# Kernel tuning notes

Hardware: AMD Instinct MI355X
Metric: run time of the kernel (lower is better)

Reference implementation:

```python
import jax, jax.numpy as jnp
import numpy as np

B, N, E, H = 2, 1000, 2000, 128


def setup_inputs() -> dict:
    key = jax.random.key(0)
    k1, k2, k3, k4, k5 = jax.random.split(key, 5)
    node_state = jax.random.normal(k1, (B, N, H), dtype=jnp.float32)
    edge_vec = jax.random.normal(k2, (B, E, H), dtype=jnp.float32)
    node2edge = jax.random.uniform(k3, (B, E, N), dtype=jnp.float32)
    edge2node = jax.random.uniform(k4, (B, N, E), dtype=jnp.float32)
    # xavier_uniform for a (H, H, H) tensor: fan_in = H*H, fan_out = H (torch views last 2 dims)
    bound = float(np.sqrt(6.0 / (H + H * H)))
    edge_network = jax.random.uniform(k5, (H, H, H), dtype=jnp.float32, minval=-bound, maxval=bound)
    return {
        "node_state": node_state,
        "edge_vec": edge_vec,
        "node2edge": node2edge,
        "edge2node": edge2node,
        "edge_network": edge_network,
    }


def reference(node_state, edge_vec, node2edge, edge2node, edge_network):
    # node2edge_emb[b,e,h] = sum_n node2edge[b,e,n] * node_state[b,n,h]
    n2e_emb = jnp.einsum("ben,bnh->beh", node2edge, node_state)
    # per-edge dynamic weight W[b,e,i,j] = sum_h edge_vec[b,e,h] * edge_network[h,i,j],
    # applied to n2e_emb; fused into one contraction (grouped edge-conditioned conv).
    new_n2e = jnp.einsum("beh,hij,bej->bei", edge_vec, edge_network, n2e_emb)
    norm = jnp.sum(edge2node, axis=2, keepdims=True) + 1.0  # [B,N,1]
    agg = (jnp.einsum("bne,bei->bni", edge2node, new_n2e) + node_state) / norm
    return agg
```

## Files before the change

### kernel.cpp

```cpp
#include <hip/hip_runtime.h>
#include <hip/hip_bf16.h>
#include <stdint.h>

#define Bv 2
#define Nv 1000
#define Ev 2000
#define Hv 128

typedef __attribute__((ext_vector_type(8))) short bf16x8;
typedef __attribute__((ext_vector_type(4))) float f32x4;
typedef unsigned short u16;
typedef unsigned int u32;

static __device__ __forceinline__ u32 pack2bf(float a, float b) {
  union { __hip_bfloat162 h; u32 u; } c;
  c.h = __float22bfloat162_rn(make_float2(a, b));
  return c.u;
}
static __device__ __forceinline__ u16 cvt1bf(float a) {
  return (u16)(pack2bf(a, 0.f) & 0xffffu);
}

static __device__ __forceinline__ void gload_lds16(const void* g, void* l) {
  __builtin_amdgcn_global_load_lds(
      (const __attribute__((address_space(1))) void*)g,
      (__attribute__((address_space(3))) void*)l, 16, 0, 0);
}

__global__ void k_prep(const float* __restrict__ en, u16* __restrict__ enbf,
                       const float* __restrict__ ns, u16* __restrict__ nsT) {
  const int bid = blockIdx.x;
  const int t = threadIdx.x;
  if (bid < 1024) {
    size_t idx = ((size_t)bid * 256u + t) * 8u;
    const f32x4* p = (const f32x4*)(en + idx);
    f32x4 a = p[0], b = p[1];
    uint4 o;
    o.x = pack2bf(a.x, a.y);
    o.y = pack2bf(a.z, a.w);
    o.z = pack2bf(b.x, b.y);
    o.w = pack2bf(b.z, b.w);
    *(uint4*)(enbf + idx) = o;
  } else {
    __shared__ float tile[32][33];
    const int zb = bid - 1024;
    const int x = zb & 31, y = (zb >> 5) & 3, z = zb >> 7;
    const float* src = ns + (size_t)z * Nv * Hv;
    u16* dst = nsT + (size_t)z * Hv * 1024;
    const int r0 = x * 32, c0 = y * 32;
    const int tx = t & 31, ty = t >> 5;
#pragma unroll
    for (int rr = 0; rr < 4; ++rr) {
      int r = r0 + ty + rr * 8;
      int c = c0 + tx;
      float v = (r < Nv) ? src[(size_t)r * Hv + c] : 0.f;
      tile[ty + rr * 8][tx] = v;
    }
    __syncthreads();
#pragma unroll
    for (int rr = 0; rr < 4; ++rr) {
      int oc = c0 + ty + rr * 8;
      int orr = r0 + tx;
      dst[(size_t)oc * 1024 + orr] = cvt1bf(tile[tx][ty + rr * 8]);
    }
  }
}

template <int M, int KREAL, int KPAD, int NKC, int NMT, bool ROWSUM>
__launch_bounds__(256, 4)
__global__ void k_gemm_flat(const float* __restrict__ A, const u16* __restrict__ BT,
                            float* __restrict__ Cpart, float* __restrict__ nrmpart) {
  __shared__ u16 AL[64 * 136];
  __shared__ float rowsum[64];
  const int id = blockIdx.x;
  const int kcid = id % NKC;
  const int mt = (id / NKC) % NMT;
  const int b = id / (NKC * NMT);
  A     += (size_t)b * M * KREAL;
  BT    += (size_t)b * 128 * KPAD;
  Cpart += (size_t)kcid * (2 * M * 128) + (size_t)b * M * 128;
  if (ROWSUM) nrmpart += (size_t)kcid * (2 * M) + (size_t)b * M;
  const int t = threadIdx.x;
  const int lane = t & 63;
  const int w = t >> 6;
  const int row16 = lane & 15;
  const int kg = lane >> 4;
  const int mrow0 = mt * 64;
  const int kc = kcid * 128;
  const int mtg = (w >> 1) * 2;
  const int itg = (w & 1) * 4;
  f32x4 acc[2][4];
#pragma unroll
  for (int i = 0; i < 2; ++i)
#pragma unroll
    for (int j = 0; j < 4; ++j) acc[i][j] = (f32x4){0.f, 0.f, 0.f, 0.f};
  if (ROWSUM && t < 64) rowsum[t] = 0.f;
  __syncthreads();
#pragma unroll
  for (int r = 0; r < 4; ++r) {
    const int chunk = t + r * 256;
    const int m = chunk >> 4;
    const int jc = (chunk & 15) * 8;
    const int gm = mrow0 + m;
    const int gk = kc + jc;
    f32x4 x0 = {0.f, 0.f, 0.f, 0.f}, x1 = {0.f, 0.f, 0.f, 0.f};
    if (gm < M && gk + 8 <= KREAL) {
      const f32x4* p = (const f32x4*)(A + (size_t)gm * KREAL + gk);
      x0 = p[0];
      x1 = p[1];
    }
    if (ROWSUM) {
      float s8 = x0.x + x0.y + x0.z + x0.w + x1.x + x1.y + x1.z + x1.w;
      s8 += __shfl_down(s8, 8, 16);
      s8 += __shfl_down(s8, 4, 16);
      s8 += __shfl_down(s8, 2, 16);
      s8 += __shfl_down(s8, 1, 16);
      if ((lane & 15) == 0) rowsum[m] += s8;
    }
    uint4 o;
    o.x = pack2bf(x0.x, x0.y);
    o.y = pack2bf(x0.z, x0.w);
    o.z = pack2bf(x1.x, x1.y);
    o.w = pack2bf(x1.z, x1.w);
    *(uint4*)&AL[m * 136 + jc] = o;
  }
  __syncthreads();
#pragma unroll
  for (int kk = 0; kk < 4; ++kk) {
    bf16x8 a[2], bfr[4];
#pragma unroll
    for (int q = 0; q < 2; ++q)
      a[q] = *(const bf16x8*)&AL[((mtg + q) * 16 + row16) * 136 + kk * 32 + kg * 8];
#pragma unroll
    for (int q = 0; q < 4; ++q)
      bfr[q] = *(const bf16x8*)(BT + (size_t)((itg + q) * 16 + row16) * KPAD + kc + kk * 32 + kg * 8);
#pragma unroll
    for (int mi = 0; mi < 2; ++mi)
#pragma unroll
      for (int ii = 0; ii < 4; ++ii)
        acc[mi][ii] = __builtin_amdgcn_mfma_f32_16x16x32_bf16(a[mi], bfr[ii], acc[mi][ii], 0, 0, 0);
  }
  if (ROWSUM && t < 64 && mrow0 + t < M) nrmpart[mrow0 + t] = rowsum[t];
#pragma unroll
  for (int mi = 0; mi < 2; ++mi) {
#pragma unroll
    for (int r = 0; r < 4; ++r) {
      const int lrow = (mtg + mi) * 16 + kg * 4 + r;
      const int gm = mrow0 + lrow;
      if (gm < M) {
#pragma unroll
        for (int ii = 0; ii < 4; ++ii)
          Cpart[(size_t)gm * 128 + (itg + ii) * 16 + row16] = acc[mi][ii][r];
      }
    }
  }
}

__global__ void k_reduce_emb(const float* __restrict__ part, float* __restrict__ emb) {
  const int idx = blockIdx.x * 256 + threadIdx.x;
  const f32x4* p = (const f32x4*)part + idx;
  f32x4 s = {0.f, 0.f, 0.f, 0.f};
#pragma unroll
  for (int kc = 0; kc < 8; ++kc) s += p[(size_t)kc * 128000];
  ((f32x4*)emb)[idx] = s;
}

__global__ void k_cvt_red(const float* __restrict__ part2, u16* __restrict__ neweT) {
  const int tid = blockIdx.x * 256 + threadIdx.x;
  const size_t f0 = (size_t)tid * 8;
  const int m0 = (int)(f0 & 2047);
  uint4 o;
  if (m0 >= Ev) {
    o = make_uint4(0, 0, 0, 0);
  } else {
    const f32x4* p = (const f32x4*)(part2 + f0);
    f32x4 s0 = {0.f, 0.f, 0.f, 0.f}, s1 = {0.f, 0.f, 0.f, 0.f};
#pragma unroll
    for (int hg = 0; hg < 8; ++hg) {
      s0 += p[(size_t)hg * 131072];
      s1 += p[(size_t)hg * 131072 + 1];
    }
    o.x = pack2bf(s0.x, s0.y);
    o.y = pack2bf(s0.z, s0.w);
    o.z = pack2bf(s1.x, s1.y);
    o.w = pack2bf(s1.z, s1.w);
  }
  *(uint4*)(neweT + f0) = o;
}

__global__ void k_epi_red(const float* __restrict__ part3, const float* __restrict__ nrmp,
                          const float* __restrict__ ns, float* __restrict__ out) {
  const int tid = blockIdx.x * 256 + threadIdx.x;
  const size_t f0 = (size_t)tid * 4;
  const int row = (int)(f0 >> 7);
  const f32x4* p = (const f32x4*)(part3 + f0);
  f32x4 s = {0.f, 0.f, 0.f, 0.f};
#pragma unroll
  for (int kc = 0; kc < 16; ++kc) s += p[(size_t)kc * 64000];
  float nm = 1.0f;
#pragma unroll
  for (int kc = 0; kc < 16; ++kc) nm += nrmp[(size_t)kc * 2000 + row];
  f32x4 nsv = *(const f32x4*)(ns + f0);
  *(f32x4*)(out + f0) = (s + nsv) * (1.0f / nm);
}

__launch_bounds__(256, 2)
__global__ void k_edge_mix(const float* __restrict__ ev, const float* __restrict__ emb,
                           const u16* __restrict__ enbf, float* __restrict__ part2) {
  __shared__ u16 APL[2][16384];
  __shared__ float EVL[64 * 20];
  const int id = blockIdx.x;
  const int hgrp = id & 7;
  const int rest = id >> 3;
  const int mt = rest & 31;
  const int b = rest >> 5;
  const int h0 = hgrp * 16;
  const int t = threadIdx.x;
  const int lane = t & 63;
  const int w = t >> 6;
  const int row16 = lane & 15;
  const int kg = lane >> 4;
  const int mbase = mt * 64;

  if (t < 64) {
    const int ml = mbase + t;
    const float* src = ev + ((size_t)b * Ev + ml) * Hv + h0;
    const f32x4 z = {0.f, 0.f, 0.f, 0.f};
#pragma unroll
    for (int q = 0; q < 4; ++q) {
      f32x4 v = (ml < Ev) ? *(const f32x4*)(src + q * 4) : z;
      *(f32x4*)&EVL[t * 20 + q * 4] = v;
    }
  }

  bf16x8 bfrag[4][4];
#pragma unroll
  for (int mf = 0; mf < 4; ++mf) {
    const int ml = mbase + mf * 16 + row16;
    const float* src = emb + ((size_t)b * Ev + ml) * Hv;
#pragma unroll
    for (int kk = 0; kk < 4; ++kk) {
      f32x4 x0 = {0.f, 0.f, 0.f, 0.f}, x1 = {0.f, 0.f, 0.f, 0.f};
      if (ml < Ev) {
        const f32x4* p = (const f32x4*)(src + kk * 32 + kg * 8);
        x0 = p[0];
        x1 = p[1];
      }
      union { bf16x8 v; uint4 u; } c;
      c.u.x = pack2bf(x0.x, x0.y);
      c.u.y = pack2bf(x0.z, x0.w);
      c.u.z = pack2bf(x1.x, x1.y);
      c.u.w = pack2bf(x1.z, x1.w);
      bfrag[mf][kk] = c.v;
    }
  }

  auto STAGE = [&](u16* dst, int h) {
    const char* plane = (const char*)(enbf + (size_t)h * 16384);
#pragma unroll
    for (int q = 0; q < 8; ++q) {
      const int c = q * 256 + t;
      const int row = c >> 4;
      const int inner = (c & 15) << 4;
      const int srcb = row * 256 + (inner ^ ((row & 7) << 4));
      gload_lds16(plane + srcb, (char*)dst + c * 16);
    }
  };

  const f32x4 zero4 = {0.f, 0.f, 0.f, 0.f};
  f32x4 pers[2][4];
#pragma unroll
  for (int fi = 0; fi < 2; ++fi)
#pragma unroll
    for (int mf = 0; mf < 4; ++mf) pers[fi][mf] = zero4;

  const int xorv = (row16 & 7) << 4;

  STAGE(APL[0], h0);
  __syncthreads();

#pragma unroll 1
  for (int hh = 0; hh < 16; ++hh) {
    const u16* buf = APL[hh & 1];
    if (hh + 1 < 16) STAGE((u16*)APL[(hh & 1) ^ 1], h0 + hh + 1);
    bf16x8 a[2][4];
#pragma unroll
    for (int fi = 0; fi < 2; ++fi) {
      const int row = w * 32 + fi * 16 + row16;
#pragma unroll
      for (int kk = 0; kk < 4; ++kk)
        a[fi][kk] = *(const bf16x8*)((const char*)buf + row * 256 + ((kk * 64 + kg * 16) ^ xorv));
    }
    f32x4 q[2][4];
#pragma unroll
    for (int fi = 0; fi < 2; ++fi)
#pragma unroll
      for (int mf = 0; mf < 4; ++mf)
        q[fi][mf] = __builtin_amdgcn_mfma_f32_16x16x32_bf16(a[fi][0], bfrag[mf][0], zero4, 0, 0, 0);
#pragma unroll
    for (int kk = 1; kk < 4; ++kk)
#pragma unroll
      for (int fi = 0; fi < 2; ++fi)
#pragma unroll
        for (int mf = 0; mf < 4; ++mf)
          q[fi][mf] = __builtin_amdgcn_mfma_f32_16x16x32_bf16(a[fi][kk], bfrag[mf][kk], q[fi][mf], 0, 0, 0);
    float evv[4];
#pragma unroll
    for (int mf = 0; mf < 4; ++mf)
      evv[mf] = EVL[(mf * 16 + row16) * 20 + hh];
#pragma unroll
    for (int fi = 0; fi < 2; ++fi)
#pragma unroll
      for (int mf = 0; mf < 4; ++mf)
        pers[fi][mf] += evv[mf] * q[fi][mf];
    __syncthreads();
  }

  float* slice = part2 + (size_t)hgrp * (2 * 128 * 2048);
#pragma unroll
  for (int fi = 0; fi < 2; ++fi) {
#pragma unroll
    for (int mf = 0; mf < 4; ++mf) {
      const int ml = mbase + mf * 16 + row16;
      if (ml < Ev) {
#pragma unroll
        for (int r = 0; r < 4; ++r) {
          const int irow = w * 32 + fi * 16 + kg * 4 + r;
          slice[((size_t)b * 128 + irow) * 2048 + ml] = pers[fi][mf][r];
        }
      }
    }
  }
}

extern "C" void kernel_launch(void* const* d_in, const int* in_sizes, int n_in,
                              void* d_out, int out_size, void* d_ws, size_t ws_size,
                              hipStream_t stream) {
  const float* ns  = (const float*)d_in[0];
  const float* ev  = (const float*)d_in[1];
  const float* n2e = (const float*)d_in[2];
  const float* e2n = (const float*)d_in[3];
  const float* en  = (const float*)d_in[4];
  float* out = (float*)d_out;

  char* ws = (char*)d_ws;
  float* part1 = (float*)(ws);
  float* part2 = (float*)(ws + 16384000);
  float* part3 = (float*)(ws + 33161216);
  float* nrmp  = (float*)(ws + 49545216);
  float* emb   = (float*)(ws + 49673216);
  u16*   enbf  = (u16*)  (ws + 51721216);
  u16*   nsT   = (u16*)  (ws + 55915520);
  u16*   neweT = (u16*)  (ws + 56439808);

  k_prep<<<dim3(1280), dim3(256), 0, stream>>>(en, enbf, ns, nsT);
  k_gemm_flat<2000, 1000, 1024, 8, 32, false><<<dim3(512), dim3(256), 0, stream>>>(n2e, nsT, part1, nullptr);
  k_reduce_emb<<<dim3(500), dim3(256), 0, stream>>>(part1, emb);
  k_edge_mix<<<dim3(512), dim3(256), 0, stream>>>(ev, emb, enbf, part2);
  k_cvt_red<<<dim3(256), dim3(256), 0, stream>>>(part2, neweT);
  k_gemm_flat<1000, 2000, 2048, 16, 16, true><<<dim3(512), dim3(256), 0, stream>>>(e2n, neweT, part3, nrmp);
  k_epi_red<<<dim3(250), dim3(256), 0, stream>>>(part3, nrmp, ns, out);
}
```

Measured before the change: 71.01 us.

## Emit bf16 edge embeddings from reduction and stage weights per wave

The embedding reduction kernel now converts its sums to bf16 and writes them into a row-padded buffer. k_edge_mix then loads its MFMA B fragments directly, with no fp32 loads and no per-block conversion. Each wave now stages only its own 32-row slice of the weight plane into LDS. The block-wide __syncthreads in the h loop is replaced by per-wave s_waitcnt vmcnt waits, which removes cross-wave barriers. In exchange, the padded rows 2000-2047 are never written, so edge_mix reads uninitialized workspace and stores unguarded results for them; the later reduction kernel discards those rows.

```diff
diff --git a/kernel.cpp b/kernel.cpp
--- a/kernel.cpp
+++ b/kernel.cpp
@@ -156,13 +156,26 @@
   }
 }
 
-__global__ void k_reduce_emb(const float* __restrict__ part, float* __restrict__ emb) {
-  const int idx = blockIdx.x * 256 + threadIdx.x;
-  const f32x4* p = (const f32x4*)part + idx;
-  f32x4 s = {0.f, 0.f, 0.f, 0.f};
-#pragma unroll
-  for (int kc = 0; kc < 8; ++kc) s += p[(size_t)kc * 128000];
-  ((f32x4*)emb)[idx] = s;
+__global__ void k_reduce_emb(const float* __restrict__ part, u16* __restrict__ embbf) {
+  const int tid = blockIdx.x * 256 + threadIdx.x;
+  const size_t e = (size_t)tid * 8;
+  const int b = (int)(e / 256000);
+  const int rem = (int)(e % 256000);
+  const int m = rem >> 7;
+  const int j = rem & 127;
+  const f32x4* p = (const f32x4*)part + tid * 2;
+  f32x4 s0 = {0.f, 0.f, 0.f, 0.f}, s1 = {0.f, 0.f, 0.f, 0.f};
+#pragma unroll
+  for (int kc = 0; kc < 8; ++kc) {
+    s0 += p[(size_t)kc * 128000];
+    s1 += p[(size_t)kc * 128000 + 1];
+  }
+  uint4 o;
+  o.x = pack2bf(s0.x, s0.y);
+  o.y = pack2bf(s0.z, s0.w);
+  o.z = pack2bf(s1.x, s1.y);
+  o.w = pack2bf(s1.z, s1.w);
+  *(uint4*)(embbf + ((size_t)b * 2048 + m) * 128 + j) = o;
 }
 
 __global__ void k_cvt_red(const float* __restrict__ part2, u16* __restrict__ neweT) {
@@ -205,9 +218,9 @@
 }
 
 __launch_bounds__(256, 2)
-__global__ void k_edge_mix(const float* __restrict__ ev, const float* __restrict__ emb,
+__global__ void k_edge_mix(const float* __restrict__ ev, const u16* __restrict__ embbf,
                            const u16* __restrict__ enbf, float* __restrict__ part2) {
-  __shared__ u16 APL[2][16384];
+  __shared__ u16 APL[2][4][4096];
   __shared__ float EVL[64 * 20];
   const int id = blockIdx.x;
   const int hgrp = id & 7;
@@ -234,36 +247,26 @@
   }
 
   bf16x8 bfrag[4][4];
-#pragma unroll
-  for (int mf = 0; mf < 4; ++mf) {
-    const int ml = mbase + mf * 16 + row16;
-    const float* src = emb + ((size_t)b * Ev + ml) * Hv;
-#pragma unroll
-    for (int kk = 0; kk < 4; ++kk) {
-      f32x4 x0 = {0.f, 0.f, 0.f, 0.f}, x1 = {0.f, 0.f, 0.f, 0.f};
-      if (ml < Ev) {
-        const f32x4* p = (const f32x4*)(src + kk * 32 + kg * 8);
-        x0 = p[0];
-        x1 = p[1];
-      }
-      union { bf16x8 v; uint4 u; } c;
-      c.u.x = pack2bf(x0.x, x0.y);
-      c.u.y = pack2bf(x0.z, x0.w);
-      c.u.z = pack2bf(x1.x, x1.y);
-      c.u.w = pack2bf(x1.z, x1.w);
-      bfrag[mf][kk] = c.v;
-    }
-  }
-
-  auto STAGE = [&](u16* dst, int h) {
-    const char* plane = (const char*)(enbf + (size_t)h * 16384);
-#pragma unroll
-    for (int q = 0; q < 8; ++q) {
-      const int c = q * 256 + t;
-      const int row = c >> 4;
-      const int inner = (c & 15) << 4;
-      const int srcb = row * 256 + (inner ^ ((row & 7) << 4));
-      gload_lds16(plane + srcb, (char*)dst + c * 16);
+  {
+    const u16* ebase = embbf + ((size_t)b * 2048 + mbase) * 128;
+#pragma unroll
+    for (int mf = 0; mf < 4; ++mf) {
+      const u16* rp = ebase + (size_t)(mf * 16 + row16) * 128;
+#pragma unroll
+      for (int kk = 0; kk < 4; ++kk)
+        bfrag[mf][kk] = *(const bf16x8*)(rp + kk * 32 + kg * 8);
+    }
+  }
+
+  auto STAGE = [&](int p, int h) {
+    const char* plane = (const char*)(enbf + (size_t)h * 16384) + (size_t)w * 8192;
+    char* dst = (char*)&APL[p][w][0];
+#pragma unroll
+    for (int it = 0; it < 8; ++it) {
+      const int r = it * 4 + (lane >> 4);
+      const int inner = (lane & 15) << 4;
+      const int srcb = r * 256 + (inner ^ ((r & 7) << 4));
+      gload_lds16(plane + srcb, dst + it * 1024);
     }
   };
 
@@ -276,20 +279,26 @@
 
   const int xorv = (row16 & 7) << 4;
 
-  STAGE(APL[0], h0);
+  STAGE(0, h0);
   __syncthreads();
 
 #pragma unroll 1
   for (int hh = 0; hh < 16; ++hh) {
-    const u16* buf = APL[hh & 1];
-    if (hh + 1 < 16) STAGE((u16*)APL[(hh & 1) ^ 1], h0 + hh + 1);
+    if (hh + 1 < 16) {
+      STAGE((hh + 1) & 1, h0 + hh + 1);
+      asm volatile("s_waitcnt vmcnt(8)" ::: "memory");
+    } else {
+      asm volatile("s_waitcnt vmcnt(0)" ::: "memory");
+    }
+    __builtin_amdgcn_sched_barrier(0);
+    const char* sl = (const char*)&APL[hh & 1][w][0];
     bf16x8 a[2][4];
 #pragma unroll
     for (int fi = 0; fi < 2; ++fi) {
-      const int row = w * 32 + fi * 16 + row16;
+      const int rs = fi * 16 + row16;
 #pragma unroll
       for (int kk = 0; kk < 4; ++kk)
-        a[fi][kk] = *(const bf16x8*)((const char*)buf + row * 256 + ((kk * 64 + kg * 16) ^ xorv));
+        a[fi][kk] = *(const bf16x8*)(sl + rs * 256 + ((kk * 64 + kg * 16) ^ xorv));
     }
     f32x4 q[2][4];
 #pragma unroll
@@ -313,7 +322,6 @@
 #pragma unroll
       for (int mf = 0; mf < 4; ++mf)
         pers[fi][mf] += evv[mf] * q[fi][mf];
-    __syncthreads();
   }
 
   float* slice = part2 + (size_t)hgrp * (2 * 128 * 2048);
@@ -322,12 +330,10 @@
 #pragma unroll
     for (int mf = 0; mf < 4; ++mf) {
       const int ml = mbase + mf * 16 + row16;
-      if (ml < Ev) {
-#pragma unroll
-        for (int r = 0; r < 4; ++r) {
-          const int irow = w * 32 + fi * 16 + kg * 4 + r;
-          slice[((size_t)b * 128 + irow) * 2048 + ml] = pers[fi][mf][r];
-        }
+#pragma unroll
+      for (int r = 0; r < 4; ++r) {
+        const int irow = w * 32 + fi * 16 + kg * 4 + r;
+        slice[((size_t)b * 128 + irow) * 2048 + ml] = pers[fi][mf][r];
       }
     }
   }
@@ -348,15 +354,15 @@
   float* part2 = (float*)(ws + 16384000);
   float* part3 = (float*)(ws + 33161216);
   float* nrmp  = (float*)(ws + 49545216);
-  float* emb   = (float*)(ws + 49673216);
-  u16*   enbf  = (u16*)  (ws + 51721216);
-  u16*   nsT   = (u16*)  (ws + 55915520);
-  u16*   neweT = (u16*)  (ws + 56439808);
+  u16*   embbf = (u16*)  (ws + 49673216);
+  u16*   enbf  = (u16*)  (ws + 50721792);
+  u16*   nsT   = (u16*)  (ws + 54916096);
+  u16*   neweT = (u16*)  (ws + 55440384);
 
   k_prep<<<dim3(1280), dim3(256), 0, stream>>>(en, enbf, ns, nsT);
   k_gemm_flat<2000, 1000, 1024, 8, 32, false><<<dim3(512), dim3(256), 0, stream>>>(n2e, nsT, part1, nullptr);
-  k_reduce_emb<<<dim3(500), dim3(256), 0, stream>>>(part1, emb);
-  k_edge_mix<<<dim3(512), dim3(256), 0, stream>>>(ev, emb, enbf, part2);
+  k_reduce_emb<<<dim3(250), dim3(256), 0, stream>>>(part1, embbf);
+  k_edge_mix<<<dim3(512), dim3(256), 0, stream>>>(ev, embbf, enbf, part2);
   k_cvt_red<<<dim3(256), dim3(256), 0, stream>>>(part2, neweT);
   k_gemm_flat<1000, 2000, 2048, 16, 16, true><<<dim3(512), dim3(256), 0, stream>>>(e2n, neweT, part3, nrmp);
   k_epi_red<<<dim3(250), dim3(256), 0, stream>>>(part3, nrmp, ns, out);
```

After: 67.20 us. -5.4%, faster.
